# Optimization experiments

Measured on AMD Instinct MI355X. Metric: run time of the kernel, lower is better.

## Reference

```python
import jax, jax.numpy as jnp
import numpy as np

# Mistral-7B attention dims
B, S, D = 4, 1024, 4096
NH, NKV, HD = 32, 8, 128
SLIDING_WINDOW = 4096


def setup_inputs() -> dict:
    key = jax.random.key(0)
    ks = jax.random.split(key, 6)
    x = jax.random.normal(ks[0], (B, S, D), jnp.float32) * 0.02
    wq = jax.random.normal(ks[1], (NH * HD, D), jnp.float32) * 0.02
    wk = jax.random.normal(ks[2], (NKV * HD, D), jnp.float32) * 0.02
    wv = jax.random.normal(ks[3], (NKV * HD, D), jnp.float32) * 0.02
    wo = jax.random.normal(ks[4], (D, NH * HD), jnp.float32) * 0.02
    # RoPE frequencies (theta=10000), shape [S, HD//2]
    inv_freq = 1.0 / (10000.0 ** (jnp.arange(0, HD, 2, dtype=jnp.float32) / HD))
    angles = jnp.arange(S, dtype=jnp.float32)[:, None] * inv_freq[None, :]
    freqs_cos = jnp.cos(angles)
    freqs_sin = jnp.sin(angles)
    # sliding-window causal additive mask [S, S]
    i = jnp.arange(S)
    visible = (i[:, None] >= i[None, :]) & (i[:, None] - i[None, :] < SLIDING_WINDOW)
    mask = jnp.where(visible, 0.0, -1e9).astype(jnp.float32)
    positions = jnp.arange(S, dtype=jnp.int32)
    return {
        'x': x, 'wq': wq, 'wk': wk, 'wv': wv, 'wo': wo,
        'freqs_cos': freqs_cos, 'freqs_sin': freqs_sin,
        'mask': mask, 'positions': positions, 'seqlen': S,
    }


def _rope(t, fc, fs):
    # t: [B, S, H, HD]; fc/fs: [S, HD//2]; interleaved real/imag complex rotation
    tr = t[..., 0::2]
    ti = t[..., 1::2]
    fc = fc[None, :, None, :]
    fs = fs[None, :, None, :]
    out_r = tr * fc - ti * fs
    out_i = tr * fs + ti * fc
    return jnp.stack([out_r, out_i], axis=-1).reshape(t.shape)


def reference(x, wq, wk, wv, wo, freqs_cos, freqs_sin, mask, positions, seqlen):
    bsz = x.shape[0]
    scale = HD ** -0.5
    # QKV projections (TtLinear: y = x @ W^T, no bias)
    q = (x @ wq.T).reshape(bsz, seqlen, NH, HD)
    k = (x @ wk.T).reshape(bsz, seqlen, NKV, HD)
    v = (x @ wv.T).reshape(bsz, seqlen, NKV, HD)
    # inline rotary embedding on q, k
    q = _rope(q, freqs_cos, freqs_sin)
    k = _rope(k, freqs_cos, freqs_sin)
    # GQA: repeat_interleave kv heads (prefill path: positions.shape[0] > 1)
    rep = NH // NKV
    k = jnp.repeat(k, rep, axis=2)  # [B, S, NH, HD]
    v = jnp.repeat(v, rep, axis=2)
    scores = jnp.einsum('bqhd,bkhd->bhqk', q, k) * scale + mask[None, None]
    attn = jax.nn.softmax(scores, axis=-1)
    out = jnp.einsum('bhqk,bkhd->bqhd', attn, v).reshape(bsz, seqlen, NH * HD)
    return out @ wo.T
```

## Files before the change

kernel.cpp:

```cpp
#include <hip/hip_runtime.h>
#include <hip/hip_bf16.h>
#include <stdint.h>


typedef __bf16 bf16x8 __attribute__((ext_vector_type(8)));
typedef float floatx4 __attribute__((ext_vector_type(4)));

__device__ __forceinline__ unsigned short f2bf(float f) {
    union { float f; uint32_t u; } v; v.f = f;
    uint32_t u = v.u;
    uint32_t r = (u + 0x7FFFu + ((u >> 16) & 1u)) >> 16;
    return (unsigned short)r;
}
__device__ __forceinline__ float bf2f(unsigned short h) {
    union { uint32_t u; float f; } v; v.u = ((uint32_t)h) << 16;
    return v.f;
}

__device__ __forceinline__ void async_copy16(const void* g, void* l) {
    __builtin_amdgcn_global_load_lds(
        (const __attribute__((address_space(1))) unsigned int*)g,
        (__attribute__((address_space(3))) unsigned int*)l,
        16, 0, 0);
}

__global__ void cast_bf16_kernel(const float* __restrict__ in,
                                 unsigned short* __restrict__ out, int n4) {
    int i = blockIdx.x * blockDim.x + threadIdx.x;
    if (i >= n4) return;
    float4 v = ((const float4*)in)[i];
    ushort4 o;
    o.x = f2bf(v.x); o.y = f2bf(v.y); o.z = f2bf(v.z); o.w = f2bf(v.w);
    ((ushort4*)out)[i] = o;
}

#define GBM 128
#define GBN 128
#define GBK 64

__global__ __launch_bounds__(256)
void gemm_bt_kernel(const unsigned short* __restrict__ A,
                    const unsigned short* __restrict__ B,
                    void* __restrict__ Cout, int M, int N, int K, int out_is_bf16)
{
    __shared__ unsigned short As[GBM * GBK];
    __shared__ unsigned short Bs[GBN * GBK];

    const int tid  = threadIdx.x;
    const int lane = tid & 63;
    const int wave = tid >> 6;
    const int quad = lane >> 4;
    const int l15  = lane & 15;

    const int bm = blockIdx.y * GBM;
    const int bn = blockIdx.x * GBN;
    const int waveM = (wave >> 1) * 64;
    const int waveN = (wave & 1) * 64;

    floatx4 acc[4][4];
    #pragma unroll
    for (int i = 0; i < 4; i++)
        #pragma unroll
        for (int j = 0; j < 4; j++)
            acc[i][j] = floatx4{0.f, 0.f, 0.f, 0.f};

    const int srow = wave * 8 + (lane >> 3);
    const int gcol = (((lane & 7) ^ (lane >> 3)) << 4);
    uint8_t* AsB = (uint8_t*)As;
    uint8_t* BsB = (uint8_t*)Bs;

    for (int k0 = 0; k0 < K; k0 += GBK) {
        __syncthreads();
        const uint8_t* Ab = (const uint8_t*)A + (size_t)k0 * 2;
        const uint8_t* Bb = (const uint8_t*)B + (size_t)k0 * 2;
        #pragma unroll
        for (int i = 0; i < 4; i++) {
            int row = i * 32 + srow;
            async_copy16(Ab + (size_t)(bm + row) * K * 2 + gcol, AsB + i * 4096 + wave * 1024);
            async_copy16(Bb + (size_t)(bn + row) * K * 2 + gcol, BsB + i * 4096 + wave * 1024);
        }
        __syncthreads();

        #pragma unroll
        for (int kk = 0; kk < 2; kk++) {
            bf16x8 af[4], bfr[4];
            #pragma unroll
            for (int i = 0; i < 4; i++) {
                int row = waveM + i * 16 + l15;
                af[i] = *(const bf16x8*)(AsB + row * 128 +
                          ((((kk << 2) | quad) ^ (l15 & 7)) << 4));
            }
            #pragma unroll
            for (int j = 0; j < 4; j++) {
                int row = waveN + j * 16 + l15;
                bfr[j] = *(const bf16x8*)(BsB + row * 128 +
                          ((((kk << 2) | quad) ^ (l15 & 7)) << 4));
            }
            #pragma unroll
            for (int i = 0; i < 4; i++)
                #pragma unroll
                for (int j = 0; j < 4; j++)
                    acc[i][j] = __builtin_amdgcn_mfma_f32_16x16x32_bf16(af[i], bfr[j], acc[i][j], 0, 0, 0);
        }
    }

    const int rowBase = bm + waveM + quad * 4;
    const int colBase = bn + waveN + l15;
    if (out_is_bf16) {
        unsigned short* C = (unsigned short*)Cout;
        #pragma unroll
        for (int i = 0; i < 4; i++)
            #pragma unroll
            for (int j = 0; j < 4; j++)
                #pragma unroll
                for (int r = 0; r < 4; r++)
                    C[(size_t)(rowBase + i * 16 + r) * N + colBase + j * 16] = f2bf(acc[i][j][r]);
    } else {
        float* C = (float*)Cout;
        #pragma unroll
        for (int i = 0; i < 4; i++)
            #pragma unroll
            for (int j = 0; j < 4; j++)
                #pragma unroll
                for (int r = 0; r < 4; r++)
                    C[(size_t)(rowBase + i * 16 + r) * N + colBase + j * 16] = acc[i][j][r];
    }
}

__global__ __launch_bounds__(512, 2)
void gemm_bt_256_kernel(const unsigned short* __restrict__ A,
                        const unsigned short* __restrict__ B,
                        void* __restrict__ Cout, int M, int N, int K, int out_is_bf16)
{
    __shared__ uint8_t lds[4 * 32768];

    const int tid  = threadIdx.x;
    const int lane = tid & 63;
    const int wave = tid >> 6;
    const int quad = lane >> 4;
    const int l15  = lane & 15;
    const int wr   = wave >> 2;
    const int wc   = wave & 3;

    const int nwg = gridDim.x * gridDim.y;
    int orig = blockIdx.y * gridDim.x + blockIdx.x;
    int swzb = (nwg & 7) ? orig : ((orig & 7) * (nwg >> 3) + (orig >> 3));
    const int bm = (swzb / gridDim.x) * 256;
    const int bn = (swzb % gridDim.x) * 256;

    const int srow = wave * 32 + (lane >> 2);
    const int sg   = (((lane & 3) ^ ((lane >> 3) & 3)) << 4);
    const uint8_t* Ar0 = (const uint8_t*)(A + (size_t)(bm + srow) * K) + sg;
    const uint8_t* Ar1 = (const uint8_t*)(A + (size_t)(bm + srow + 16) * K) + sg;
    const uint8_t* Br0 = (const uint8_t*)(B + (size_t)(bn + srow) * K) + sg;
    const uint8_t* Br1 = (const uint8_t*)(B + (size_t)(bn + srow + 16) * K) + sg;
    const int ldsA0 = wave * 2048;
    const int ldsA1 = wave * 2048 + 1024;

    const int rsw  = (quad ^ ((l15 >> 1) & 3)) << 4;
    const int aoff = (wr * 128 + l15) * 64 + rsw;
    const int boff = 16384 + (wc * 64 + l15) * 64 + rsw;

    floatx4 acc[8][4];
    #pragma unroll
    for (int m = 0; m < 8; m++)
        #pragma unroll
        for (int n = 0; n < 4; n++)
            acc[m][n] = floatx4{0.f, 0.f, 0.f, 0.f};

    auto stage = [&](int t) {
        uint8_t* buf = lds + (size_t)(t & 3) * 32768;
        const size_t koff = (size_t)t * 64;
        async_copy16(Ar0 + koff, buf + ldsA0);
        async_copy16(Ar1 + koff, buf + ldsA1);
        async_copy16(Br0 + koff, buf + 16384 + ldsA0);
        async_copy16(Br1 + koff, buf + 16384 + ldsA1);
    };

    stage(0); stage(1); stage(2);

    const int NT = K >> 5;
    for (int t = 0; t < NT; ++t) {
        if (t < NT - 2)
            asm volatile("s_waitcnt vmcnt(8)\n\ts_barrier" ::: "memory");
        else if (t == NT - 2)
            asm volatile("s_waitcnt vmcnt(4)\n\ts_barrier" ::: "memory");
        else
            asm volatile("s_waitcnt vmcnt(0)\n\ts_barrier" ::: "memory");

        if (t + 3 < NT) stage(t + 3);

        const uint8_t* buf = lds + (size_t)(t & 3) * 32768;
        bf16x8 a0[4], b0[4], a1[4];
        #pragma unroll
        for (int m = 0; m < 4; m++) a0[m] = *(const bf16x8*)(buf + aoff + m * 1024);
        #pragma unroll
        for (int n = 0; n < 4; n++) b0[n] = *(const bf16x8*)(buf + boff + n * 1024);
        __builtin_amdgcn_s_setprio(1);
        #pragma unroll
        for (int m = 0; m < 4; m++)
            #pragma unroll
            for (int n = 0; n < 4; n++)
                acc[m][n] = __builtin_amdgcn_mfma_f32_16x16x32_bf16(a0[m], b0[n], acc[m][n], 0, 0, 0);
        __builtin_amdgcn_s_setprio(0);
        #pragma unroll
        for (int m = 0; m < 4; m++) a1[m] = *(const bf16x8*)(buf + aoff + (4 + m) * 1024);
        __builtin_amdgcn_s_setprio(1);
        #pragma unroll
        for (int m = 0; m < 4; m++)
            #pragma unroll
            for (int n = 0; n < 4; n++)
                acc[4 + m][n] = __builtin_amdgcn_mfma_f32_16x16x32_bf16(a1[m], b0[n], acc[4 + m][n], 0, 0, 0);
        __builtin_amdgcn_s_setprio(0);
    }

    const int rowBase = bm + wr * 128 + quad * 4;
    const int colBase = bn + wc * 64 + l15;
    if (out_is_bf16) {
        unsigned short* C = (unsigned short*)Cout;
        #pragma unroll
        for (int m = 0; m < 8; m++)
            #pragma unroll
            for (int n = 0; n < 4; n++)
                #pragma unroll
                for (int r = 0; r < 4; r++)
                    C[(size_t)(rowBase + m * 16 + r) * N + colBase + n * 16] = f2bf(acc[m][n][r]);
    } else {
        float* C = (float*)Cout;
        #pragma unroll
        for (int m = 0; m < 8; m++)
            #pragma unroll
            for (int n = 0; n < 4; n++)
                #pragma unroll
                for (int r = 0; r < 4; r++)
                    C[(size_t)(rowBase + m * 16 + r) * N + colBase + n * 16] = acc[m][n][r];
    }
}

__global__ void rope_kernel(unsigned short* __restrict__ t,
                            const float* __restrict__ fc,
                            const float* __restrict__ fs,
                            int nh, int total_pairs) {
    int idx = blockIdx.x * blockDim.x + threadIdx.x;
    if (idx >= total_pairs) return;
    int j   = idx & 63;
    int tmp = idx >> 6;
    int s   = (tmp / nh) & 1023;
    float c  = fc[s * 64 + j];
    float sn = fs[s * 64 + j];
    size_t base = (size_t)tmp * 128 + j * 2;
    float tr = bf2f(t[base]), ti = bf2f(t[base + 1]);
    t[base]     = f2bf(tr * c - ti * sn);
    t[base + 1] = f2bf(tr * sn + ti * c);
}

#define AS_  1024
#define AHD 128
#define ANH 32
#define ANKV 8

__global__ __launch_bounds__(512, 4)
void attn_kernel(const unsigned short* __restrict__ Q,
                 const unsigned short* __restrict__ Kk,
                 const unsigned short* __restrict__ Vt,
                 unsigned short* __restrict__ O)
{
    __shared__ uint8_t lds[81920];

    const int tid  = threadIdx.x;
    const int lane = tid & 63;
    const int wave = tid >> 6;
    const int quad = lane >> 4;
    const int l15  = lane & 15;

    const int bid = blockIdx.x;
    const int qt2 = 7 - (bid & 7);
    const int h   = (bid >> 3) & 31;
    const int b   = bid >> 8;
    const int hk  = h >> 2;
    const int q0  = qt2 * 128;

    uint8_t* ldsK = lds;
    uint8_t* ldsV = lds + 32768;
    uint8_t* Ps   = lds + 65536 + wave * 2048;

    const int krow0 = (2 * wave + 0) * 4 + (lane >> 4);
    const int krow1 = (2 * wave + 1) * 4 + (lane >> 4);
    const int kg0 = ((lane & 15) ^ (0 + (lane >> 4))) * 8;
    const int kg1 = ((lane & 15) ^ (4 + (lane >> 4))) * 8;
    const unsigned short* Kg0 = Kk + ((size_t)(b * AS_ + krow0) * ANKV + hk) * AHD + kg0;
    const unsigned short* Kg1 = Kk + ((size_t)(b * AS_ + krow1) * ANKV + hk) * AHD + kg1;
    const int vrow0 = (2 * wave + 0) * 8 + (lane >> 3);
    const int vrow1 = (2 * wave + 1) * 8 + (lane >> 3);
    const int vg = ((lane & 7) ^ (lane >> 3)) * 8;
    const unsigned short* Vg0 = Vt + (size_t)(hk * AHD + vrow0) * (4 * AS_) + b * AS_ + vg;
    const unsigned short* Vg1 = Vt + (size_t)(hk * AHD + vrow1) * (4 * AS_) + b * AS_ + vg;

    auto stage = [&](int t) {
        uint8_t* kb_ = ldsK + (t & 1) * 16384;
        uint8_t* vb_ = ldsV + (t & 1) * 16384;
        async_copy16(Kg0 + (size_t)t * 65536, kb_ + (2 * wave + 0) * 1024);
        async_copy16(Kg1 + (size_t)t * 65536, kb_ + (2 * wave + 1) * 1024);
        async_copy16(Vg0 + t * 64, vb_ + (2 * wave + 0) * 1024);
        async_copy16(Vg1 + t * 64, vb_ + (2 * wave + 1) * 1024);
    };

    bf16x8 aq[4];
    {
        const int qrow = q0 + wave * 16 + l15;
        const unsigned short* src = Q + ((size_t)(b * AS_ + qrow) * ANH + h) * AHD;
        #pragma unroll
        for (int kk = 0; kk < 4; kk++)
            aq[kk] = *(const bf16x8*)(src + kk * 32 + quad * 8);
    }

    float lsum[4];
    #pragma unroll
    for (int r = 0; r < 4; r++) lsum[r] = 0.0f;
    floatx4 o[8];
    #pragma unroll
    for (int d = 0; d < 8; d++) o[d] = floatx4{0.f, 0.f, 0.f, 0.f};

    const float scale = 0.08838834764831845f;
    const int wMaxKt = (q0 + wave * 16 + 15) >> 6;
    const int ktMax  = (q0 + 127) >> 6;

    stage(0);
    const int swz = (l15 & 7) << 4;

    for (int kt = 0; kt <= ktMax; ++kt) {
        if (kt < ktMax) {
            stage(kt + 1);
            asm volatile("s_waitcnt vmcnt(4)\n\ts_barrier" ::: "memory");
        } else {
            asm volatile("s_waitcnt vmcnt(0)\n\ts_barrier" ::: "memory");
        }

        if (kt <= wMaxKt) {
            const uint8_t* kb_ = ldsK + (kt & 1) * 16384;
            const uint8_t* vb_ = ldsV + (kt & 1) * 16384;

            floatx4 sc[4];
            #pragma unroll
            for (int j = 0; j < 4; j++) sc[j] = floatx4{0.f, 0.f, 0.f, 0.f};
            __builtin_amdgcn_s_setprio(1);
            #pragma unroll
            for (int j = 0; j < 4; j++)
                #pragma unroll
                for (int kk = 0; kk < 4; kk++) {
                    bf16x8 bk = *(const bf16x8*)(kb_ + (j * 16 + l15) * 256 +
                                  (((kk * 4 + quad) << 4) ^ swz));
                    sc[j] = __builtin_amdgcn_mfma_f32_16x16x32_bf16(aq[kk], bk, sc[j], 0, 0, 0);
                }
            __builtin_amdgcn_s_setprio(0);

            #pragma unroll
            for (int r = 0; r < 4; r++) {
                const int row  = quad * 4 + r;
                const int qrow = q0 + wave * 16 + row;
                const bool needMask = (kt * 64 + 63 > qrow);
                float acc = 0.0f;
                #pragma unroll
                for (int j = 0; j < 4; j++) {
                    float e = __expf(sc[j][r] * scale);
                    if (needMask) {
                        int key = kt * 64 + j * 16 + l15;
                        if (key > qrow) e = 0.0f;
                    }
                    acc += e;
                    int g = (j * 2 + (l15 >> 3)) ^ (row & 7);
                    *(unsigned short*)(Ps + row * 128 + (g << 4) + (l15 & 7) * 2) = f2bf(e);
                }
                lsum[r] += acc;
            }

            __builtin_amdgcn_s_setprio(1);
            #pragma unroll
            for (int kk = 0; kk < 2; kk++) {
                bf16x8 ap = *(const bf16x8*)(Ps + l15 * 128 +
                              (((kk * 4 + quad) << 4) ^ swz));
                #pragma unroll
                for (int d = 0; d < 8; d++) {
                    bf16x8 bv = *(const bf16x8*)(vb_ + (d * 16 + l15) * 128 +
                                  (((kk * 4 + quad) << 4) ^ swz));
                    o[d] = __builtin_amdgcn_mfma_f32_16x16x32_bf16(ap, bv, o[d], 0, 0, 0);
                }
            }
            __builtin_amdgcn_s_setprio(0);
        }

        asm volatile("s_barrier" ::: "memory");
    }

    #pragma unroll
    for (int r = 0; r < 4; r++) {
        float s = lsum[r];
        #pragma unroll
        for (int off = 1; off < 16; off <<= 1)
            s += __shfl_xor(s, off, 64);
        float inv = 1.0f / s;
        int qrow = q0 + wave * 16 + quad * 4 + r;
        unsigned short* dst = O + ((size_t)(b * AS_ + qrow) * ANH + h) * AHD;
        #pragma unroll
        for (int d = 0; d < 8; d++)
            dst[d * 16 + l15] = f2bf(o[d][r] * inv);
    }
}

extern "C" void kernel_launch(void* const* d_in, const int* in_sizes, int n_in,
                              void* d_out, int out_size, void* d_ws, size_t ws_size,
                              hipStream_t stream)
{
    const float* x  = (const float*)d_in[0];
    const float* wq = (const float*)d_in[1];
    const float* wk = (const float*)d_in[2];
    const float* wv = (const float*)d_in[3];
    const float* wo = (const float*)d_in[4];
    const float* fc = (const float*)d_in[5];
    const float* fs = (const float*)d_in[6];

    const int B = 4, S = 1024, D = 4096, NH = 32, NKV = 8, HD = 128;
    const int M    = B * S;
    const int NQ   = NH * HD;
    const int NKVD = NKV * HD;

    unsigned short* ws = (unsigned short*)d_ws;
    size_t off = 0;
    unsigned short* xb  = ws + off; off += (size_t)M * D;
    unsigned short* wqb = ws + off; off += (size_t)NQ * D;
    unsigned short* wkb = ws + off; off += (size_t)NKVD * D;
    unsigned short* wvb = ws + off; off += (size_t)NKVD * D;
    unsigned short* wob = ws + off; off += (size_t)D * NQ;
    unsigned short* qb  = ws + off; off += (size_t)M * NQ;
    unsigned short* kb  = ws + off; off += (size_t)M * NKVD;
    unsigned short* vtb = ws + off; off += (size_t)NKVD * M;
    unsigned short* aob = ws + off; off += (size_t)M * NQ;

    {
        struct { const float* src; unsigned short* dst; size_t n; } jobs[5] = {
            { x,  xb,  (size_t)M * D },
            { wq, wqb, (size_t)NQ * D },
            { wk, wkb, (size_t)NKVD * D },
            { wv, wvb, (size_t)NKVD * D },
            { wo, wob, (size_t)D * NQ },
        };
        for (int i = 0; i < 5; i++) {
            int n4 = (int)(jobs[i].n / 4);
            cast_bf16_kernel<<<(n4 + 255) / 256, 256, 0, stream>>>(jobs[i].src, jobs[i].dst, n4);
        }
    }

    gemm_bt_256_kernel<<<dim3(NQ / 256,  M / 256), 512, 0, stream>>>(xb,  wqb, qb,  M,   NQ, D, 1);
    gemm_bt_kernel<<<dim3(NKVD / GBN, M / GBM), 256, 0, stream>>>(xb,  wkb, kb,  M, NKVD, D, 1);
    gemm_bt_kernel<<<dim3(M / GBN, NKVD / GBM), 256, 0, stream>>>(wvb, xb,  vtb, NKVD, M, D, 1);

    {
        int pq = M * NH * (HD / 2);
        rope_kernel<<<(pq + 255) / 256, 256, 0, stream>>>(qb, fc, fs, NH, pq);
        int pk = M * NKV * (HD / 2);
        rope_kernel<<<(pk + 255) / 256, 256, 0, stream>>>(kb, fc, fs, NKV, pk);
    }

    attn_kernel<<<B * NH * (S / 128), 512, 0, stream>>>(qb, kb, vtb, aob);

    gemm_bt_256_kernel<<<dim3(D / 256, M / 256), 512, 0, stream>>>(aob, wob, d_out, M, D, NQ, 0);
}
```

Baseline: 741.3 us.

## Shrink big GEMM tile to 128x256 with 3-stage LDS pipeline

Reduces the large bf16 GEMM block tile from 256x256 to 128x256 and halves per-wave accumulators. The LDS ring drops from four 32KB slots to three 24KB slots with prefetch depth two, and launch bounds rise to allow more resident blocks. For the M=4096, N=4096 GEMMs this doubles the grid from 256 to 512 blocks, which should improve occupancy and CU coverage. In exchange each block reuses operands less, so global/L2 traffic per FLOP goes up, and the shallower prefetch hides less latency.

Result: slower. 774.6 us (+4.5%).

```diff
diff --git a/kernel.cpp b/kernel.cpp
--- a/kernel.cpp
+++ b/kernel.cpp
@@ -127,12 +127,16 @@
     }
 }
 
-__global__ __launch_bounds__(512, 2)
+#define WBM 128
+#define WBN 256
+#define WSLOT 24576
+
+__global__ __launch_bounds__(512, 4)
 void gemm_bt_256_kernel(const unsigned short* __restrict__ A,
                         const unsigned short* __restrict__ B,
                         void* __restrict__ Cout, int M, int N, int K, int out_is_bf16)
 {
-    __shared__ uint8_t lds[4 * 32768];
+    __shared__ uint8_t lds[3 * WSLOT];
 
     const int tid  = threadIdx.x;
     const int lane = tid & 63;
@@ -145,95 +149,87 @@
     const int nwg = gridDim.x * gridDim.y;
     int orig = blockIdx.y * gridDim.x + blockIdx.x;
     int swzb = (nwg & 7) ? orig : ((orig & 7) * (nwg >> 3) + (orig >> 3));
-    const int bm = (swzb / gridDim.x) * 256;
-    const int bn = (swzb % gridDim.x) * 256;
-
-    const int srow = wave * 32 + (lane >> 2);
-    const int sg   = (((lane & 3) ^ ((lane >> 3) & 3)) << 4);
-    const uint8_t* Ar0 = (const uint8_t*)(A + (size_t)(bm + srow) * K) + sg;
-    const uint8_t* Ar1 = (const uint8_t*)(A + (size_t)(bm + srow + 16) * K) + sg;
-    const uint8_t* Br0 = (const uint8_t*)(B + (size_t)(bn + srow) * K) + sg;
-    const uint8_t* Br1 = (const uint8_t*)(B + (size_t)(bn + srow + 16) * K) + sg;
-    const int ldsA0 = wave * 2048;
-    const int ldsA1 = wave * 2048 + 1024;
+    const int bm = (swzb / gridDim.x) * WBM;
+    const int bn = (swzb % gridDim.x) * WBN;
+
+    const int sgr = lane >> 2;
+    const int sg  = (((lane & 3) ^ ((lane >> 3) & 3)) << 4);
+    const uint8_t* Ag  = (const uint8_t*)(A + (size_t)(bm + wave * 16 + sgr) * K) + sg;
+    const uint8_t* Bg0 = (const uint8_t*)(B + (size_t)(bn + wave * 32 + sgr) * K) + sg;
+    const uint8_t* Bg1 = (const uint8_t*)(B + (size_t)(bn + wave * 32 + 16 + sgr) * K) + sg;
+    const int ldsA  = wave * 1024;
+    const int ldsB0 = 8192 + wave * 2048;
+    const int ldsB1 = ldsB0 + 1024;
 
     const int rsw  = (quad ^ ((l15 >> 1) & 3)) << 4;
-    const int aoff = (wr * 128 + l15) * 64 + rsw;
-    const int boff = 16384 + (wc * 64 + l15) * 64 + rsw;
-
-    floatx4 acc[8][4];
+    const int aoff = (wr * 64 + l15) * 64 + rsw;
+    const int boff = 8192 + (wc * 64 + l15) * 64 + rsw;
+
+    floatx4 acc[4][4];
     #pragma unroll
-    for (int m = 0; m < 8; m++)
+    for (int m = 0; m < 4; m++)
         #pragma unroll
         for (int n = 0; n < 4; n++)
             acc[m][n] = floatx4{0.f, 0.f, 0.f, 0.f};
 
-    auto stage = [&](int t) {
-        uint8_t* buf = lds + (size_t)(t & 3) * 32768;
+    auto stage = [&](int t, uint8_t* buf) {
         const size_t koff = (size_t)t * 64;
-        async_copy16(Ar0 + koff, buf + ldsA0);
-        async_copy16(Ar1 + koff, buf + ldsA1);
-        async_copy16(Br0 + koff, buf + 16384 + ldsA0);
-        async_copy16(Br1 + koff, buf + 16384 + ldsA1);
+        async_copy16(Ag  + koff, buf + ldsA);
+        async_copy16(Bg0 + koff, buf + ldsB0);
+        async_copy16(Bg1 + koff, buf + ldsB1);
     };
 
-    stage(0); stage(1); stage(2);
-
     const int NT = K >> 5;
+    stage(0, lds);
+    if (NT > 1) stage(1, lds + WSLOT);
+
+    int cur = 0;
     for (int t = 0; t < NT; ++t) {
-        if (t < NT - 2)
-            asm volatile("s_waitcnt vmcnt(8)\n\ts_barrier" ::: "memory");
-        else if (t == NT - 2)
-            asm volatile("s_waitcnt vmcnt(4)\n\ts_barrier" ::: "memory");
+        if (t + 1 < NT)
+            asm volatile("s_waitcnt vmcnt(3)\n\ts_barrier" ::: "memory");
         else
             asm volatile("s_waitcnt vmcnt(0)\n\ts_barrier" ::: "memory");
 
-        if (t + 3 < NT) stage(t + 3);
-
-        const uint8_t* buf = lds + (size_t)(t & 3) * 32768;
-        bf16x8 a0[4], b0[4], a1[4];
-        #pragma unroll
-        for (int m = 0; m < 4; m++) a0[m] = *(const bf16x8*)(buf + aoff + m * 1024);
-        #pragma unroll
-        for (int n = 0; n < 4; n++) b0[n] = *(const bf16x8*)(buf + boff + n * 1024);
+        int nxt2 = cur + 2; if (nxt2 >= 3) nxt2 -= 3;
+        if (t + 2 < NT) stage(t + 2, lds + nxt2 * WSLOT);
+
+        const uint8_t* buf = lds + cur * WSLOT;
+        bf16x8 a[4], b[4];
+        #pragma unroll
+        for (int m = 0; m < 4; m++) a[m] = *(const bf16x8*)(buf + aoff + m * 1024);
+        #pragma unroll
+        for (int n = 0; n < 4; n++) b[n] = *(const bf16x8*)(buf + boff + n * 1024);
         __builtin_amdgcn_s_setprio(1);
         #pragma unroll
         for (int m = 0; m < 4; m++)
             #pragma unroll
             for (int n = 0; n < 4; n++)
-                acc[m][n] = __builtin_amdgcn_mfma_f32_16x16x32_bf16(a0[m], b0[n], acc[m][n], 0, 0, 0);
+                acc[m][n] = __builtin_amdgcn_mfma_f32_16x16x32_bf16(a[m], b[n], acc[m][n], 0, 0, 0);
         __builtin_amdgcn_s_setprio(0);
-        #pragma unroll
-        for (int m = 0; m < 4; m++) a1[m] = *(const bf16x8*)(buf + aoff + (4 + m) * 1024);
-        __builtin_amdgcn_s_setprio(1);
-        #pragma unroll
-        for (int m = 0; m < 4; m++)
-            #pragma unroll
-            for (int n = 0; n < 4; n++)
-                acc[4 + m][n] = __builtin_amdgcn_mfma_f32_16x16x32_bf16(a1[m], b0[n], acc[4 + m][n], 0, 0, 0);
-        __builtin_amdgcn_s_setprio(0);
-    }
-
-    const int rowBase = bm + wr * 128 + quad * 4;
+
+        cur = (cur == 2) ? 0 : cur + 1;
+    }
+
+    const int rowBase = bm + wr * 64 + quad * 4;
     const int colBase = bn + wc * 64 + l15;
     if (out_is_bf16) {
         unsigned short* C = (unsigned short*)Cout;
         #pragma unroll
-        for (int m = 0; m < 8; m++)
-            #pragma unroll
-            for (int n = 0; n < 4; n++)
+        for (int i = 0; i < 4; i++)
+            #pragma unroll
+            for (int j = 0; j < 4; j++)
                 #pragma unroll
                 for (int r = 0; r < 4; r++)
-                    C[(size_t)(rowBase + m * 16 + r) * N + colBase + n * 16] = f2bf(acc[m][n][r]);
+                    C[(size_t)(rowBase + i * 16 + r) * N + colBase + j * 16] = f2bf(acc[i][j][r]);
     } else {
         float* C = (float*)Cout;
         #pragma unroll
-        for (int m = 0; m < 8; m++)
-            #pragma unroll
-            for (int n = 0; n < 4; n++)
+        for (int i = 0; i < 4; i++)
+            #pragma unroll
+            for (int j = 0; j < 4; j++)
                 #pragma unroll
                 for (int r = 0; r < 4; r++)
-                    C[(size_t)(rowBase + m * 16 + r) * N + colBase + n * 16] = acc[m][n][r];
+                    C[(size_t)(rowBase + i * 16 + r) * N + colBase + j * 16] = acc[i][j][r];
     }
 }
 
@@ -450,7 +446,7 @@
         }
     }
 
-    gemm_bt_256_kernel<<<dim3(NQ / 256,  M / 256), 512, 0, stream>>>(xb,  wqb, qb,  M,   NQ, D, 1);
+    gemm_bt_256_kernel<<<dim3(NQ / WBN, M / WBM), 512, 0, stream>>>(xb,  wqb, qb,  M,   NQ, D, 1);
     gemm_bt_kernel<<<dim3(NKVD / GBN, M / GBM), 256, 0, stream>>>(xb,  wkb, kb,  M, NKVD, D, 1);
     gemm_bt_kernel<<<dim3(M / GBN, NKVD / GBM), 256, 0, stream>>>(wvb, xb,  vtb, NKVD, M, D, 1);
 
@@ -463,5 +459,5 @@
 
     attn_kernel<<<B * NH * (S / 128), 512, 0, stream>>>(qb, kb, vtb, aob);
 
-    gemm_bt_256_kernel<<<dim3(D / 256, M / 256), 512, 0, stream>>>(aob, wob, d_out, M, D, NQ, 0);
-}
+    gemm_bt_256_kernel<<<dim3(D / WBN, M / WBM), 512, 0, stream>>>(aob, wob, d_out, M, D, NQ, 0);
+}
```

## Restructure 256x256 GEMM to K=64 double-buffered tiles with quadrant-staged loads

Applied to the files above, without the earlier changes.

The main 256x256 bf16 GEMM kernel moves from a 4-stage ring of K=32 tiles to a 2-stage double buffer of K=64 tiles with a new XOR swizzle. Each iteration is split into four MFMA quadrants, and loads for the next tiles are issued piecewise between them, with barriers separating the phases. The goal is finer overlap of global-to-LDS copies with MFMA work and fewer loop iterations. In exchange there are more barriers per iteration and less prefetch depth, which can stall if memory latency is not hidden.

After: 741.8 us. No clear change (+0.1%).

```diff
diff --git a/kernel.cpp b/kernel.cpp
--- a/kernel.cpp
+++ b/kernel.cpp
@@ -132,7 +132,7 @@
                         const unsigned short* __restrict__ B,
                         void* __restrict__ Cout, int M, int N, int K, int out_is_bf16)
 {
-    __shared__ uint8_t lds[4 * 32768];
+    __shared__ uint8_t lds[2 * 65536];
 
     const int tid  = threadIdx.x;
     const int lane = tid & 63;
@@ -148,18 +148,51 @@
     const int bm = (swzb / gridDim.x) * 256;
     const int bn = (swzb % gridDim.x) * 256;
 
-    const int srow = wave * 32 + (lane >> 2);
-    const int sg   = (((lane & 3) ^ ((lane >> 3) & 3)) << 4);
-    const uint8_t* Ar0 = (const uint8_t*)(A + (size_t)(bm + srow) * K) + sg;
-    const uint8_t* Ar1 = (const uint8_t*)(A + (size_t)(bm + srow + 16) * K) + sg;
-    const uint8_t* Br0 = (const uint8_t*)(B + (size_t)(bn + srow) * K) + sg;
-    const uint8_t* Br1 = (const uint8_t*)(B + (size_t)(bn + srow + 16) * K) + sg;
-    const int ldsA0 = wave * 2048;
-    const int ldsA1 = wave * 2048 + 1024;
-
-    const int rsw  = (quad ^ ((l15 >> 1) & 3)) << 4;
-    const int aoff = (wr * 128 + l15) * 64 + rsw;
-    const int boff = 16384 + (wc * 64 + l15) * 64 + rsw;
+    const int srw = lane >> 3;
+    const int sgb = (((lane & 7) ^ (lane >> 3)) << 4);
+    const int a0r0 = wave * 8,       a0r1 = 128 + wave * 8;
+    const int a1r0 = 64 + wave * 8,  a1r1 = 192 + wave * 8;
+    const int b0r0 = (wave >> 2) * 64 + (wave & 3) * 8;
+    const int b0r1 = ((wave + 8) >> 2) * 64 + (wave & 3) * 8;
+    const int b1r0 = b0r0 + 32,      b1r1 = b0r1 + 32;
+    const uint8_t* pA00 = (const uint8_t*)A + (size_t)(bm + a0r0 + srw) * K * 2 + sgb;
+    const uint8_t* pA01 = (const uint8_t*)A + (size_t)(bm + a0r1 + srw) * K * 2 + sgb;
+    const uint8_t* pA10 = (const uint8_t*)A + (size_t)(bm + a1r0 + srw) * K * 2 + sgb;
+    const uint8_t* pA11 = (const uint8_t*)A + (size_t)(bm + a1r1 + srw) * K * 2 + sgb;
+    const uint8_t* pB00 = (const uint8_t*)B + (size_t)(bn + b0r0 + srw) * K * 2 + sgb;
+    const uint8_t* pB01 = (const uint8_t*)B + (size_t)(bn + b0r1 + srw) * K * 2 + sgb;
+    const uint8_t* pB10 = (const uint8_t*)B + (size_t)(bn + b1r0 + srw) * K * 2 + sgb;
+    const uint8_t* pB11 = (const uint8_t*)B + (size_t)(bn + b1r1 + srw) * K * 2 + sgb;
+
+    auto stA0 = [&](int t) {
+        uint8_t* d = lds + (t & 1) * 65536;
+        const size_t ko = (size_t)t * 128;
+        async_copy16(pA00 + ko, d + a0r0 * 128);
+        async_copy16(pA01 + ko, d + a0r1 * 128);
+    };
+    auto stA1 = [&](int t) {
+        uint8_t* d = lds + (t & 1) * 65536;
+        const size_t ko = (size_t)t * 128;
+        async_copy16(pA10 + ko, d + a1r0 * 128);
+        async_copy16(pA11 + ko, d + a1r1 * 128);
+    };
+    auto stB0 = [&](int t) {
+        uint8_t* d = lds + (t & 1) * 65536 + 32768;
+        const size_t ko = (size_t)t * 128;
+        async_copy16(pB00 + ko, d + b0r0 * 128);
+        async_copy16(pB01 + ko, d + b0r1 * 128);
+    };
+    auto stB1 = [&](int t) {
+        uint8_t* d = lds + (t & 1) * 65536 + 32768;
+        const size_t ko = (size_t)t * 128;
+        async_copy16(pB10 + ko, d + b1r0 * 128);
+        async_copy16(pB11 + ko, d + b1r1 * 128);
+    };
+
+    const int rs0 = ((0 + quad) ^ (l15 & 7)) << 4;
+    const int rs1 = ((4 + quad) ^ (l15 & 7)) << 4;
+    const int arow = (wr * 128 + l15) * 128;
+    const int brow = 32768 + (wc * 64 + l15) * 128;
 
     floatx4 acc[8][4];
     #pragma unroll
@@ -168,50 +201,101 @@
         for (int n = 0; n < 4; n++)
             acc[m][n] = floatx4{0.f, 0.f, 0.f, 0.f};
 
-    auto stage = [&](int t) {
-        uint8_t* buf = lds + (size_t)(t & 3) * 32768;
-        const size_t koff = (size_t)t * 64;
-        async_copy16(Ar0 + koff, buf + ldsA0);
-        async_copy16(Ar1 + koff, buf + ldsA1);
-        async_copy16(Br0 + koff, buf + 16384 + ldsA0);
-        async_copy16(Br1 + koff, buf + 16384 + ldsA1);
-    };
-
-    stage(0); stage(1); stage(2);
-
-    const int NT = K >> 5;
+    const int NT = K >> 6;
+
+    stA0(0); stB0(0); stB1(0); stA1(0);
+    if (NT > 1) {
+        stA0(1); stB0(1); stB1(1);
+        asm volatile("s_waitcnt vmcnt(6)\n\ts_barrier" ::: "memory");
+    } else {
+        asm volatile("s_waitcnt vmcnt(0)\n\ts_barrier" ::: "memory");
+    }
+
     for (int t = 0; t < NT; ++t) {
-        if (t < NT - 2)
-            asm volatile("s_waitcnt vmcnt(8)\n\ts_barrier" ::: "memory");
-        else if (t == NT - 2)
-            asm volatile("s_waitcnt vmcnt(4)\n\ts_barrier" ::: "memory");
-        else
+        const uint8_t* buf = lds + (t & 1) * 65536;
+        bf16x8 a[4][2], a2[4][2], b0[2][2], b1[2][2];
+
+        if (t + 1 < NT) stA1(t + 1);
+        #pragma unroll
+        for (int f = 0; f < 4; f++) {
+            a[f][0] = *(const bf16x8*)(buf + arow + f * 2048 + rs0);
+            a[f][1] = *(const bf16x8*)(buf + arow + f * 2048 + rs1);
+        }
+        #pragma unroll
+        for (int n = 0; n < 2; n++) {
+            b0[n][0] = *(const bf16x8*)(buf + brow + n * 2048 + rs0);
+            b0[n][1] = *(const bf16x8*)(buf + brow + n * 2048 + rs1);
+        }
+        asm volatile("s_waitcnt lgkmcnt(8)" ::: "memory");
+        asm volatile("s_barrier" ::: "memory");
+        asm volatile("s_waitcnt lgkmcnt(0)" ::: "memory");
+        __builtin_amdgcn_s_setprio(1);
+        #pragma unroll
+        for (int f = 0; f < 4; f++)
+            #pragma unroll
+            for (int n = 0; n < 2; n++)
+                #pragma unroll
+                for (int kk = 0; kk < 2; kk++)
+                    acc[f][n] = __builtin_amdgcn_mfma_f32_16x16x32_bf16(a[f][kk], b0[n][kk], acc[f][n], 0, 0, 0);
+        __builtin_amdgcn_s_setprio(0);
+        asm volatile("s_barrier" ::: "memory");
+
+        if (t + 2 < NT) stA0(t + 2);
+        #pragma unroll
+        for (int n = 0; n < 2; n++) {
+            b1[n][0] = *(const bf16x8*)(buf + brow + 4096 + n * 2048 + rs0);
+            b1[n][1] = *(const bf16x8*)(buf + brow + 4096 + n * 2048 + rs1);
+        }
+        asm volatile("s_barrier" ::: "memory");
+        asm volatile("s_waitcnt lgkmcnt(0)" ::: "memory");
+        __builtin_amdgcn_s_setprio(1);
+        #pragma unroll
+        for (int f = 0; f < 4; f++)
+            #pragma unroll
+            for (int n = 0; n < 2; n++)
+                #pragma unroll
+                for (int kk = 0; kk < 2; kk++)
+                    acc[f][2 + n] = __builtin_amdgcn_mfma_f32_16x16x32_bf16(a[f][kk], b1[n][kk], acc[f][2 + n], 0, 0, 0);
+        __builtin_amdgcn_s_setprio(0);
+        asm volatile("s_barrier" ::: "memory");
+
+        if (t + 2 < NT) stB0(t + 2);
+        #pragma unroll
+        for (int f = 0; f < 4; f++) {
+            a2[f][0] = *(const bf16x8*)(buf + arow + 8192 + f * 2048 + rs0);
+            a2[f][1] = *(const bf16x8*)(buf + arow + 8192 + f * 2048 + rs1);
+        }
+        asm volatile("s_barrier" ::: "memory");
+        asm volatile("s_waitcnt lgkmcnt(0)" ::: "memory");
+        __builtin_amdgcn_s_setprio(1);
+        #pragma unroll
+        for (int f = 0; f < 4; f++)
+            #pragma unroll
+            for (int n = 0; n < 2; n++)
+                #pragma unroll
+                for (int kk = 0; kk < 2; kk++)
+                    acc[4 + f][2 + n] = __builtin_amdgcn_mfma_f32_16x16x32_bf16(a2[f][kk], b1[n][kk], acc[4 + f][2 + n], 0, 0, 0);
+        __builtin_amdgcn_s_setprio(0);
+        asm volatile("s_barrier" ::: "memory");
+
+        if (t + 2 < NT) {
+            stB1(t + 2);
+            asm volatile("s_waitcnt vmcnt(6)\n\ts_barrier" ::: "memory");
+        } else if (t + 1 < NT) {
             asm volatile("s_waitcnt vmcnt(0)\n\ts_barrier" ::: "memory");
-
-        if (t + 3 < NT) stage(t + 3);
-
-        const uint8_t* buf = lds + (size_t)(t & 3) * 32768;
-        bf16x8 a0[4], b0[4], a1[4];
-        #pragma unroll
-        for (int m = 0; m < 4; m++) a0[m] = *(const bf16x8*)(buf + aoff + m * 1024);
-        #pragma unroll
-        for (int n = 0; n < 4; n++) b0[n] = *(const bf16x8*)(buf + boff + n * 1024);
+        } else {
+            asm volatile("s_barrier" ::: "memory");
+        }
         __builtin_amdgcn_s_setprio(1);
         #pragma unroll
-        for (int m = 0; m < 4; m++)
-            #pragma unroll
-            for (int n = 0; n < 4; n++)
-                acc[m][n] = __builtin_amdgcn_mfma_f32_16x16x32_bf16(a0[m], b0[n], acc[m][n], 0, 0, 0);
+        for (int f = 0; f < 4; f++)
+            #pragma unroll
+            for (int n = 0; n < 2; n++)
+                #pragma unroll
+                for (int kk = 0; kk < 2; kk++)
+                    acc[4 + f][n] = __builtin_amdgcn_mfma_f32_16x16x32_bf16(a2[f][kk], b0[n][kk], acc[4 + f][n], 0, 0, 0);
         __builtin_amdgcn_s_setprio(0);
-        #pragma unroll
-        for (int m = 0; m < 4; m++) a1[m] = *(const bf16x8*)(buf + aoff + (4 + m) * 1024);
-        __builtin_amdgcn_s_setprio(1);
-        #pragma unroll
-        for (int m = 0; m < 4; m++)
-            #pragma unroll
-            for (int n = 0; n < 4; n++)
-                acc[4 + m][n] = __builtin_amdgcn_mfma_f32_16x16x32_bf16(a1[m], b0[n], acc[4 + m][n], 0, 0, 0);
-        __builtin_amdgcn_s_setprio(0);
+        asm volatile("s_barrier" ::: "memory");
     }
 
     const int rowBase = bm + wr * 128 + quad * 4;
```
